# Kernel tuning notes

Hardware: AMD Instinct MI355X
Metric: run time of the kernel (lower is better)

Reference implementation:

```python
import jax, jax.numpy as jnp
import numpy as np

GAMMA = 0.99
B, S, V = 16, 4096, 128
TRUNC = 11  # original code sums over t in range(seqlen - 11)


def setup_inputs() -> dict:
    key = jax.random.key(0)
    k1, k2 = jax.random.split(key)
    log_probs = jax.random.normal(k1, (S, B, V), dtype=jnp.float32)
    logits = jax.random.normal(k2, (B, S, V), dtype=jnp.float32)
    return {"log_probs": log_probs, "logits": logits}


def reference(log_probs, logits):
    # log_probs: [S, B, V] (time-major, as indexed by log_probs[t] in the original)
    # logits:    [B, S, V]
    b, s, v = logits.shape
    # gamma_t starts at gamma for t = S-1 and multiplies each backward step,
    # so r[:, t] gets weight gamma^(S - t) (absolute-position weighting).
    w = jnp.power(jnp.float32(GAMMA), (s - jnp.arange(s)).astype(jnp.float32))  # [S]
    weighted = w[None, :, None] * jax.nn.log_sigmoid(logits)  # [B, S, V]
    # R[t] = sum_{u >= t} weighted[:, u]  -> reverse cumulative sum along seq
    R = jnp.flip(jnp.cumsum(jnp.flip(weighted, axis=1), axis=1), axis=1)  # [B, S, V]
    T = s - TRUNC
    # E_R = sum_{t < T} R[:, t] * log_probs[t]  -> [B, V]
    E_R = jnp.einsum('btv,tbv->bv', R[:, :T], log_probs[:T])
    return E_R
```

## Files before the change

kernel.cpp:

```cpp
#include <hip/hip_runtime.h>

#define B 16
#define S 4096
#define V 128
#define TRUNC 11
#define T_LIM (S - TRUNC)

#define NC 256
#define CT (S / NC)

#define LOG2_GAMMA (-0.014499569695115089f)
#define INV_GAMMA 1.0101010101010102f

__device__ __forceinline__ float log_sigmoid(float x) {
    float e = __expf(-fabsf(x));
    return fminf(x, 0.0f) - __logf(1.0f + e);
}

__global__ __launch_bounds__(256) void partials_kernel(
    const float4* __restrict__ lp,
    const float4* __restrict__ lg,
    float* __restrict__ pA,
    float* __restrict__ pW,
    float* __restrict__ pL,
    int nc, int ct, int writeWL)
{
    int tid = blockIdx.x * blockDim.x + threadIdx.x;
    if (tid >= nc * (B * V / 4)) return;
    int v4 = tid & (V / 4 - 1);
    int b  = (tid >> 5) & (B - 1);
    int c  = tid >> 9;
    int t0 = c * ct;

    const float4* lp_p = lp + (size_t)t0 * (B * V / 4) + b * (V / 4) + v4;
    const float4* lg_p = lg + (size_t)b * (S * V / 4) + (size_t)t0 * (V / 4) + v4;

    float w = exp2f(LOG2_GAMMA * (float)(S - t0));

    float ax = 0.f, ay = 0.f, az = 0.f, aw = 0.f;
    float Ax = 0.f, Ay = 0.f, Az = 0.f, Aw = 0.f;
    float Wx = 0.f, Wy = 0.f, Wz = 0.f, Ww = 0.f;

    #pragma unroll 4
    for (int i = 0; i < ct; ++i) {
        int t = t0 + i;
        float4 l = lp_p[(size_t)i * (B * V / 4)];
        float4 x = lg_p[(size_t)i * (V / 4)];
        if (t < T_LIM) {
            ax += l.x; ay += l.y; az += l.z; aw += l.w;
        }
        float sx = w * log_sigmoid(x.x);
        float sy = w * log_sigmoid(x.y);
        float sz = w * log_sigmoid(x.z);
        float sw = w * log_sigmoid(x.w);
        Ax = fmaf(sx, ax, Ax);
        Ay = fmaf(sy, ay, Ay);
        Az = fmaf(sz, az, Az);
        Aw = fmaf(sw, aw, Aw);
        Wx += sx; Wy += sy; Wz += sz; Ww += sw;
        w *= INV_GAMMA;
    }

    int bv0 = b * V + v4 * 4;
    float As[4] = {Ax, Ay, Az, Aw};
    float Ws[4] = {Wx, Wy, Wz, Ww};
    float Ls[4] = {ax, ay, az, aw};
    #pragma unroll
    for (int j = 0; j < 4; ++j) {
        size_t idx = (size_t)(bv0 + j) * nc + c;
        pA[idx] = As[j];
        if (writeWL) { pW[idx] = Ws[j]; pL[idx] = Ls[j]; }
    }
}

__global__ __launch_bounds__(256) void combine_kernel(
    const float4* __restrict__ pA,
    const float4* __restrict__ pW,
    const float4* __restrict__ pL,
    float* __restrict__ out)
{
    int gtid = blockIdx.x * blockDim.x + threadIdx.x;
    int bv   = gtid >> 6;
    int lane = threadIdx.x & 63;
    if (bv >= B * V) return;

    const int nc4 = NC / 4;
    float4 A = pA[(size_t)bv * nc4 + lane];
    float4 W = pW[(size_t)bv * nc4 + lane];
    float4 L = pL[(size_t)bv * nc4 + lane];

    float p1 = L.x;
    float p2 = p1 + L.y;
    float p3 = p2 + L.z;
    float s  = p3 + L.w;

    float scan = s;
    #pragma unroll
    for (int off = 1; off < 64; off <<= 1) {
        float n = __shfl_up(scan, off, 64);
        if (lane >= off) scan += n;
    }
    float base = scan - s;

    float E = A.x + A.y + A.z + A.w;
    E = fmaf(base,      W.x, E);
    E = fmaf(base + p1, W.y, E);
    E = fmaf(base + p2, W.z, E);
    E = fmaf(base + p3, W.w, E);

    #pragma unroll
    for (int off = 32; off > 0; off >>= 1)
        E += __shfl_down(E, off, 64);

    if (lane == 0) out[bv] = E;
}

extern "C" void kernel_launch(void* const* d_in, const int* in_sizes, int n_in,
                              void* d_out, int out_size, void* d_ws, size_t ws_size,
                              hipStream_t stream)
{
    const float4* lp = (const float4*)d_in[0];
    const float4* lg = (const float4*)d_in[1];
    float* out = (float*)d_out;

    size_t per = (size_t)NC * (B * V);

    if (per * 3 * sizeof(float) > ws_size) {
        partials_kernel<<<(B * V / 4 + 255) / 256, 256, 0, stream>>>(
            lp, lg, out, nullptr, nullptr, 1, S, 0);
        return;
    }

    float* pA = (float*)d_ws;
    float* pW = pA + per;
    float* pL = pW + per;

    int threads1 = NC * (B * V / 4);
    partials_kernel<<<(threads1 + 255) / 256, 256, 0, stream>>>(
        lp, lg, pA, pW, pL, NC, CT, 1);

    int threads2 = B * V * 64;
    combine_kernel<<<(threads2 + 255) / 256, 256, 0, stream>>>(
        (const float4*)pA, (const float4*)pW, (const float4*)pL, out);
}
```

Measured before the change: 109.0 us.

## Double chunk count, preload chunk inputs into registers, interleave partials as float4

```diff
diff --git a/kernel.cpp b/kernel.cpp
--- a/kernel.cpp
+++ b/kernel.cpp
@@ -6,7 +6,7 @@
 #define TRUNC 11
 #define T_LIM (S - TRUNC)
 
-#define NC 256
+#define NC 512
 #define CT (S / NC)
 
 #define LOG2_GAMMA (-0.014499569695115089f)
@@ -17,23 +17,25 @@
     return fminf(x, 0.0f) - __logf(1.0f + e);
 }
 
-__global__ __launch_bounds__(256) void partials_kernel(
+__global__ __launch_bounds__(256, 4) void partials_kernel(
     const float4* __restrict__ lp,
     const float4* __restrict__ lg,
-    float* __restrict__ pA,
-    float* __restrict__ pW,
-    float* __restrict__ pL,
-    int nc, int ct, int writeWL)
+    float4* __restrict__ pAWL)
 {
     int tid = blockIdx.x * blockDim.x + threadIdx.x;
-    if (tid >= nc * (B * V / 4)) return;
     int v4 = tid & (V / 4 - 1);
     int b  = (tid >> 5) & (B - 1);
     int c  = tid >> 9;
-    int t0 = c * ct;
+    int t0 = c * CT;
 
     const float4* lp_p = lp + (size_t)t0 * (B * V / 4) + b * (V / 4) + v4;
     const float4* lg_p = lg + (size_t)b * (S * V / 4) + (size_t)t0 * (V / 4) + v4;
+
+    float4 Lv[CT], Gv[CT];
+    #pragma unroll
+    for (int i = 0; i < CT; ++i) Lv[i] = lp_p[(size_t)i * (B * V / 4)];
+    #pragma unroll
+    for (int i = 0; i < CT; ++i) Gv[i] = lg_p[(size_t)i * (V / 4)];
 
     float w = exp2f(LOG2_GAMMA * (float)(S - t0));
 
@@ -41,18 +43,16 @@
     float Ax = 0.f, Ay = 0.f, Az = 0.f, Aw = 0.f;
     float Wx = 0.f, Wy = 0.f, Wz = 0.f, Ww = 0.f;
 
-    #pragma unroll 4
-    for (int i = 0; i < ct; ++i) {
+    #pragma unroll
+    for (int i = 0; i < CT; ++i) {
         int t = t0 + i;
-        float4 l = lp_p[(size_t)i * (B * V / 4)];
-        float4 x = lg_p[(size_t)i * (V / 4)];
         if (t < T_LIM) {
-            ax += l.x; ay += l.y; az += l.z; aw += l.w;
+            ax += Lv[i].x; ay += Lv[i].y; az += Lv[i].z; aw += Lv[i].w;
         }
-        float sx = w * log_sigmoid(x.x);
-        float sy = w * log_sigmoid(x.y);
-        float sz = w * log_sigmoid(x.z);
-        float sw = w * log_sigmoid(x.w);
+        float sx = w * log_sigmoid(Gv[i].x);
+        float sy = w * log_sigmoid(Gv[i].y);
+        float sz = w * log_sigmoid(Gv[i].z);
+        float sw = w * log_sigmoid(Gv[i].w);
         Ax = fmaf(sx, ax, Ax);
         Ay = fmaf(sy, ay, Ay);
         Az = fmaf(sz, az, Az);
@@ -62,21 +62,18 @@
     }
 
     int bv0 = b * V + v4 * 4;
-    float As[4] = {Ax, Ay, Az, Aw};
-    float Ws[4] = {Wx, Wy, Wz, Ww};
-    float Ls[4] = {ax, ay, az, aw};
-    #pragma unroll
-    for (int j = 0; j < 4; ++j) {
-        size_t idx = (size_t)(bv0 + j) * nc + c;
-        pA[idx] = As[j];
-        if (writeWL) { pW[idx] = Ws[j]; pL[idx] = Ls[j]; }
-    }
+    float4 o0 = {Ax, Wx, ax, 0.f};
+    float4 o1 = {Ay, Wy, ay, 0.f};
+    float4 o2 = {Az, Wz, az, 0.f};
+    float4 o3 = {Aw, Ww, aw, 0.f};
+    pAWL[(size_t)(bv0 + 0) * NC + c] = o0;
+    pAWL[(size_t)(bv0 + 1) * NC + c] = o1;
+    pAWL[(size_t)(bv0 + 2) * NC + c] = o2;
+    pAWL[(size_t)(bv0 + 3) * NC + c] = o3;
 }
 
 __global__ __launch_bounds__(256) void combine_kernel(
-    const float4* __restrict__ pA,
-    const float4* __restrict__ pW,
-    const float4* __restrict__ pL,
+    const float4* __restrict__ pAWL,
     float* __restrict__ out)
 {
     int gtid = blockIdx.x * blockDim.x + threadIdx.x;
@@ -84,15 +81,15 @@
     int lane = threadIdx.x & 63;
     if (bv >= B * V) return;
 
-    const int nc4 = NC / 4;
-    float4 A = pA[(size_t)bv * nc4 + lane];
-    float4 W = pW[(size_t)bv * nc4 + lane];
-    float4 L = pL[(size_t)bv * nc4 + lane];
+    const float4* row = pAWL + (size_t)bv * NC + lane * (NC / 64);
+    float4 f[NC / 64];
+    #pragma unroll
+    for (int k = 0; k < NC / 64; ++k) f[k] = row[k];
 
-    float p1 = L.x;
-    float p2 = p1 + L.y;
-    float p3 = p2 + L.z;
-    float s  = p3 + L.w;
+    float pk[NC / 64];
+    float s = 0.f;
+    #pragma unroll
+    for (int k = 0; k < NC / 64; ++k) { pk[k] = s; s += f[k].z; }
 
     float scan = s;
     #pragma unroll
@@ -102,17 +99,47 @@
     }
     float base = scan - s;
 
-    float E = A.x + A.y + A.z + A.w;
-    E = fmaf(base,      W.x, E);
-    E = fmaf(base + p1, W.y, E);
-    E = fmaf(base + p2, W.z, E);
-    E = fmaf(base + p3, W.w, E);
+    float E = 0.f;
+    #pragma unroll
+    for (int k = 0; k < NC / 64; ++k)
+        E = fmaf(base + pk[k], f[k].y, E + f[k].x);
 
     #pragma unroll
     for (int off = 32; off > 0; off >>= 1)
         E += __shfl_down(E, off, 64);
 
     if (lane == 0) out[bv] = E;
+}
+
+__global__ void fallback_kernel(
+    const float4* __restrict__ lp,
+    const float4* __restrict__ lg,
+    float4* __restrict__ out)
+{
+    int tid = blockIdx.x * blockDim.x + threadIdx.x;
+    if (tid >= B * V / 4) return;
+    int v4 = tid & (V / 4 - 1);
+    int b  = tid >> 5;
+
+    const float4* lp_p = lp + (size_t)b * (V / 4) + v4;
+    const float4* lg_p = lg + (size_t)b * (S * V / 4) + v4;
+
+    float w = exp2f(LOG2_GAMMA * (float)S);
+    float ax = 0.f, ay = 0.f, az = 0.f, aw = 0.f;
+    float Ax = 0.f, Ay = 0.f, Az = 0.f, Aw = 0.f;
+
+    for (int t = 0; t < S; ++t) {
+        float4 l = lp_p[(size_t)t * (B * V / 4)];
+        float4 x = lg_p[(size_t)t * (V / 4)];
+        if (t < T_LIM) { ax += l.x; ay += l.y; az += l.z; aw += l.w; }
+        Ax = fmaf(w * log_sigmoid(x.x), ax, Ax);
+        Ay = fmaf(w * log_sigmoid(x.y), ay, Ay);
+        Az = fmaf(w * log_sigmoid(x.z), az, Az);
+        Aw = fmaf(w * log_sigmoid(x.w), aw, Aw);
+        w *= INV_GAMMA;
+    }
+    float4 o = {Ax, Ay, Az, Aw};
+    out[tid] = o;
 }
 
 extern "C" void kernel_launch(void* const* d_in, const int* in_sizes, int n_in,
@@ -123,23 +150,18 @@
     const float4* lg = (const float4*)d_in[1];
     float* out = (float*)d_out;
 
-    size_t per = (size_t)NC * (B * V);
-
-    if (per * 3 * sizeof(float) > ws_size) {
-        partials_kernel<<<(B * V / 4 + 255) / 256, 256, 0, stream>>>(
-            lp, lg, out, nullptr, nullptr, 1, S, 0);
+    size_t bytes = (size_t)NC * (B * V) * sizeof(float4);
+    if (bytes > ws_size) {
+        fallback_kernel<<<(B * V / 4 + 255) / 256, 256, 0, stream>>>(
+            lp, lg, (float4*)out);
         return;
     }
 
-    float* pA = (float*)d_ws;
-    float* pW = pA + per;
-    float* pL = pW + per;
+    float4* pAWL = (float4*)d_ws;
 
     int threads1 = NC * (B * V / 4);
-    partials_kernel<<<(threads1 + 255) / 256, 256, 0, stream>>>(
-        lp, lg, pA, pW, pL, NC, CT, 1);
+    partials_kernel<<<(threads1 + 255) / 256, 256, 0, stream>>>(lp, lg, pAWL);
 
     int threads2 = B * V * 64;
-    combine_kernel<<<(threads2 + 255) / 256, 256, 0, stream>>>(
-        (const float4*)pA, (const float4*)pW, (const float4*)pL, out);
+    combine_kernel<<<(threads2 + 255) / 256, 256, 0, stream>>>(pAWL, out);
 }
```

After: 110.4 us. About the same (+1.2%).
